# Kernel optimization log

Measured on AMD Instinct MI355X. Metric: run time of the kernel, lower is better.

## Reference

```python
import jax, jax.numpy as jnp
import numpy as np

B, N, D, H, DFF = 4096, 64, 256, 8, 1024
HD = D // H

def _ln(x, g, b):
    m = jnp.mean(x, axis=-1, keepdims=True)
    v = jnp.var(x, axis=-1, keepdims=True)
    return (x - m) / jnp.sqrt(v + 1e-5) * g + b


def setup_inputs() -> dict:
    key = jax.random.key(0)
    ks = jax.random.split(key, 16)
    s = jnp.float32(0.02)
    def rn(k, shape):
        return jax.random.normal(k, shape, dtype=jnp.float32) * s
    d2 = D // 2
    return {
        "x": jax.random.normal(ks[0], (B, N, 1), dtype=jnp.float32),
        "ve_w1": rn(ks[1], (1, d2)), "ve_b1": jnp.zeros((d2,), jnp.float32),
        "ve_w2": rn(ks[2], (d2, D)), "ve_b2": jnp.zeros((D,), jnp.float32),
        "pos_emb": rn(ks[3], (100, D)),
        "attn_in_w": rn(ks[4], (D, 3 * D)), "attn_in_b": jnp.zeros((3 * D,), jnp.float32),
        "attn_out_w": rn(ks[5], (D, D)), "attn_out_b": jnp.zeros((D,), jnp.float32),
        "ffn_w1": rn(ks[6], (D, DFF)), "ffn_b1": jnp.zeros((DFF,), jnp.float32),
        "ffn_w2": rn(ks[7], (DFF, D)), "ffn_b2": jnp.zeros((D,), jnp.float32),
        "ln1_g": jnp.ones((D,), jnp.float32), "ln1_b": jnp.zeros((D,), jnp.float32),
        "ln2_g": jnp.ones((D,), jnp.float32), "ln2_b": jnp.zeros((D,), jnp.float32),
        "rank_emb": rn(ks[8], (100, D)),
        "q_w": rn(ks[9], (D, D)), "q_b": jnp.zeros((D,), jnp.float32),
        "k_w": rn(ks[10], (D, D)), "k_b": jnp.zeros((D,), jnp.float32),
    }


def reference(x, ve_w1, ve_b1, ve_w2, ve_b2, pos_emb, attn_in_w, attn_in_b,
              attn_out_w, attn_out_b, ffn_w1, ffn_b1, ffn_w2, ffn_b2,
              ln1_g, ln1_b, ln2_g, ln2_b, rank_emb, q_w, q_b, k_w, k_b):
    # ---- encode ----
    v = jax.nn.relu(x @ ve_w1 + ve_b1) @ ve_w2 + ve_b2          # [B,N,D]
    h = v + pos_emb[:N][None]                                    # broadcast pos embed
    qkv = h @ attn_in_w + attn_in_b
    q, k, vv = jnp.split(qkv, 3, axis=-1)
    split_heads = lambda t: t.reshape(B, N, H, HD).transpose(0, 2, 1, 3)
    q, k, vv = split_heads(q), split_heads(k), split_heads(vv)
    scores = jnp.einsum('bhqd,bhkd->bhqk', q, k) / jnp.sqrt(jnp.float32(HD))
    attn = jax.nn.softmax(scores, axis=-1)
    ao = jnp.einsum('bhqk,bhkd->bhqd', attn, vv).transpose(0, 2, 1, 3).reshape(B, N, D)
    ao = ao @ attn_out_w + attn_out_b
    h = _ln(h + ao, ln1_g, ln1_b)
    ff = jax.nn.relu(h @ ffn_w1 + ffn_b1) @ ffn_w2 + ffn_b2
    enc = _ln(h + ff, ln2_g, ln2_b)                              # [B,N,D]

    # ---- pointer decode (greedy, coverage mask) ----
    Q = rank_emb[:N] @ q_w + q_b                                 # [N,D] rank queries
    K = enc @ k_w + k_b                                          # [B,N,D]
    base = jnp.einsum('td,bnd->tbn', Q, K)                       # [N,B,N] unmasked logits per rank
    bidx = jnp.arange(B)

    def step(mask, base_t):
        logits_t = jnp.where(mask > 0, base_t, -jnp.inf)         # masked_fill
        chosen = jnp.argmax(logits_t, axis=-1)                   # greedy pick
        mask = mask.at[bidx, chosen].set(0.0)                    # scatter mask update
        return mask, logits_t

    mask0 = jnp.ones((B, N), jnp.float32)
    _, all_logits = jax.lax.scan(step, mask0, base)              # [N,B,N]
    return all_logits.transpose(1, 0, 2)                         # [B,N,N]
```

## Files before the change

kernel.cpp:

```cpp
#include <hip/hip_runtime.h>
#include <math.h>


typedef __attribute__((ext_vector_type(8))) short bf16x8;
typedef __attribute__((ext_vector_type(4))) float f32x4;

#define NEG_FILL (-3.0e38f)

#define U_Q    0
#define U_VE   2048
#define U_QKV  6144
#define U_WO   30720
#define U_F1   38912
#define U_F2   71680
#define U_KW   104448
#define U_TOT  112640

#define SH_H  0
#define SH_A  16384
#define SH_SHORTS 32768
#define FB_FLOATS 4096
#define LDS_BYTES (SH_SHORTS*2 + FB_FLOATS*4)

__device__ __forceinline__ unsigned short f2bf(float f){
  unsigned u = __float_as_uint(f);
  return (unsigned short)((u + 0x7FFFu + ((u>>16)&1u)) >> 16);
}
__device__ __forceinline__ unsigned short f2bt(float f){
  return (unsigned short)(__float_as_uint(f) >> 16);
}
__device__ __forceinline__ float bf2f(unsigned short h){
  return __uint_as_float(((unsigned)h) << 16);
}

#define MFMA(a,b,c) __builtin_amdgcn_mfma_f32_16x16x32_bf16((a),(b),(c),0,0,0)
#define SM_SCALE 0.17677669529663687f
#define PRIO_HI() __builtin_amdgcn_s_setprio(1)
#define PRIO_LO() __builtin_amdgcn_s_setprio(0)

__global__ void __launch_bounds__(256) prep_q(const float* __restrict__ rank_emb,
                                              const float* __restrict__ q_w,
                                              const float* __restrict__ q_b,
                                              short* __restrict__ wsp) {
    int t = blockIdx.x;
    int c = threadIdx.x;
    float acc = q_b[c];
    for (int d = 0; d < 256; d += 4) {
        acc += rank_emb[t*256 + d + 0] * q_w[(d+0)*256 + c]
             + rank_emb[t*256 + d + 1] * q_w[(d+1)*256 + c]
             + rank_emb[t*256 + d + 2] * q_w[(d+2)*256 + c]
             + rank_emb[t*256 + d + 3] * q_w[(d+3)*256 + c];
    }
    int kb = c >> 5, lane = ((c>>3)&3)*16 + (t&15), j = c & 7;
    int u = ((t>>4)*8 + kb)*64 + lane;
    wsp[(U_Q + u)*8 + j] = (short)f2bf(acc);
}

__global__ void __launch_bounds__(256) prep_w(const float* __restrict__ ve_w2,
                                              const float* __restrict__ attn_in_w,
                                              const float* __restrict__ attn_out_w,
                                              const float* __restrict__ ffn_w1,
                                              const float* __restrict__ ffn_w2,
                                              const float* __restrict__ k_w,
                                              short* __restrict__ wsp) {
    int r = blockIdx.x*256 + threadIdx.x;
    const float* w; int N, K, base;
    if (r < 4096)                { w = ve_w2;      N = 256;  K = 128;  base = U_VE;  }
    else if ((r -= 4096)  < 24576) { w = attn_in_w;  N = 768;  K = 256;  base = U_QKV; }
    else if ((r -= 24576) < 8192)  { w = attn_out_w; N = 256;  K = 256;  base = U_WO;  }
    else if ((r -= 8192)  < 32768) { w = ffn_w1;     N = 1024; K = 256;  base = U_F1;  }
    else if ((r -= 32768) < 32768) { w = ffn_w2;     N = 256;  K = 1024; base = U_F2;  }
    else     { r -= 32768;           w = k_w;        N = 256;  K = 256;  base = U_KW;  }
    int KB = K >> 5;
    int lane = r & 63;
    int kb   = (r >> 6) % KB;
    int nt   = r / (64 * KB);
    int n  = nt*16 + (lane & 15);
    int k0 = kb*32 + (lane >> 4)*8;
    bf16x8 hv;
#pragma unroll
    for (int j = 0; j < 8; j++) hv[j] = (short)f2bf(w[(size_t)(k0 + j)*N + n]);
    *(bf16x8*)&wsp[(size_t)(base + r) * 8] = hv;
}

__global__ void __launch_bounds__(512, 4) fused_kernel(
    const float* __restrict__ x,
    const float* __restrict__ ve_w1, const float* __restrict__ ve_b1,
    const float* __restrict__ ve_b2,
    const float* __restrict__ pos_emb,
    const float* __restrict__ attn_in_b,
    const float* __restrict__ attn_out_b,
    const float* __restrict__ ffn_b1, const float* __restrict__ ffn_b2,
    const float* __restrict__ ln1_g, const float* __restrict__ ln1_b,
    const float* __restrict__ ln2_g, const float* __restrict__ ln2_b,
    const float* __restrict__ k_b,
    const short* __restrict__ wsp,
    float* __restrict__ out)
{
    extern __shared__ short sm[];
    float* smf  = (float*)(sm + SH_SHORTS);
    float* SB   = smf;

    const int tid  = threadIdx.x;
    const int b    = blockIdx.x;
    const int w    = tid >> 6;
    const int lane = tid & 63;
    const int quad = lane >> 4;
    const int lcol = lane & 15;

    const bf16x8* wsv = (const bf16x8*)wsp;
    const bf16x8* HFu = (const bf16x8*)&sm[SH_H];
    bf16x8* HFw = (bf16x8*)&sm[SH_H];

#pragma unroll
    for (int i = 0; i < 2; i++) {
        int u = tid + i*512;
        int l3 = u & 63, kb = (u >> 6) & 3, mt = u >> 8;
        int m  = mt*16 + (l3 & 15);
        int k0 = kb*32 + (l3 >> 4)*8;
        float xv = x[b*64 + m];
        bf16x8 hv;
#pragma unroll
        for (int j = 0; j < 8; j++) {
            float f = xv * ve_w1[k0 + j] + ve_b1[k0 + j];
            hv[j] = (short)f2bt(f > 0.f ? f : 0.f);
        }
        *(bf16x8*)&sm[SH_A + u*8] = hv;
    }
    __syncthreads();

    {
        f32x4 acc[2][4];
#pragma unroll
        for (int s = 0; s < 2; s++)
#pragma unroll
            for (int mi = 0; mi < 4; mi++) acc[s][mi] = (f32x4){0.f,0.f,0.f,0.f};
        PRIO_HI();
#pragma unroll
        for (int kb = 0; kb < 4; kb++) {
            bf16x8 bh0 = wsv[U_VE + ((w    )*4+kb)*64 + lane];
            bf16x8 bh1 = wsv[U_VE + ((w + 8)*4+kb)*64 + lane];
#pragma unroll
            for (int mi = 0; mi < 4; mi++) {
                bf16x8 ah = *(const bf16x8*)&sm[SH_A + ((mi*4+kb)*64 + lane)*8];
                acc[0][mi] = MFMA(ah, bh0, acc[0][mi]);
                acc[1][mi] = MFMA(ah, bh1, acc[1][mi]);
            }
        }
        PRIO_LO();
        __syncthreads();
#pragma unroll
        for (int s = 0; s < 2; s++) {
            int n = (w + s*8)*16 + lcol;
#pragma unroll
            for (int mi = 0; mi < 4; mi++)
#pragma unroll
                for (int reg = 0; reg < 4; reg++) {
                    int m = mi*16 + quad*4 + reg;
                    float val = acc[s][mi][reg] + ve_b2[n] + pos_emb[m*256 + n];
                    int kb2 = n >> 5, l2 = ((n>>3)&3)*16 + (m&15), j2 = n & 7;
                    sm[SH_H + ((mi*8 + kb2)*64 + l2)*8 + j2] = (short)f2bt(val);
                }
        }
    }
    __syncthreads();

    f32x4 aoacc[2][4];
#pragma unroll
    for (int s = 0; s < 2; s++)
#pragma unroll
        for (int mi = 0; mi < 4; mi++) aoacc[s][mi] = (f32x4){0.f,0.f,0.f,0.f};

    const int il = w & 3;
    const int eo = il >> 1, ch = il & 1;

    auto qkv_phase = [&](int p) {
        int ntv = 32 + 4*p + il;
        if (w < 4) {
            int ntg = 4*p + il;
            f32x4 acc[4];
#pragma unroll
            for (int mi = 0; mi < 4; mi++) acc[mi] = (f32x4){0.f,0.f,0.f,0.f};
            PRIO_HI();
#pragma unroll
            for (int kb = 0; kb < 8; kb++) {
                bf16x8 bh = wsv[U_QKV + (ntg*8+kb)*64 + lane];
#pragma unroll
                for (int mi = 0; mi < 4; mi++)
                    acc[mi] = MFMA(HFu[(mi*8+kb)*64 + lane], bh, acc[mi]);
            }
            PRIO_LO();
#pragma unroll
            for (int mi = 0; mi < 4; mi++)
#pragma unroll
                for (int reg = 0; reg < 4; reg++) {
                    int m  = mi*16 + quad*4 + reg;
                    int cc = ch*16 + lcol;
                    short hv = (short)f2bt(acc[mi][reg] + attn_in_b[ntg*16 + lcol]);
                    int l2 = ((cc>>3)&3)*16 + (m&15), j2 = cc & 7;
                    sm[SH_A + eo*2048 + (mi*64 + l2)*8 + j2] = hv;
                }
            f32x4 va[2];
            va[0] = (f32x4){0.f,0.f,0.f,0.f}; va[1] = (f32x4){0.f,0.f,0.f,0.f};
            PRIO_HI();
#pragma unroll
            for (int kb = 0; kb < 8; kb++) {
                bf16x8 bh = wsv[U_QKV + (ntv*8+kb)*64 + lane];
                va[0] = MFMA(HFu[(0*8+kb)*64 + lane], bh, va[0]);
                va[1] = MFMA(HFu[(1*8+kb)*64 + lane], bh, va[1]);
            }
            PRIO_LO();
#pragma unroll
            for (int mi = 0; mi < 2; mi++)
#pragma unroll
                for (int reg = 0; reg < 4; reg++) {
                    int m  = mi*16 + quad*4 + reg;
                    int cc = ch*16 + lcol;
                    short hv = (short)f2bt(va[mi][reg] + attn_in_b[ntv*16 + lcol]);
                    int kb2 = m >> 5;
                    int l2 = ((m>>3)&3)*16 + lcol, j2 = m & 7;
                    sm[SH_A + 8192 + eo*2048 + ((ch*2 + kb2)*64 + l2)*8 + j2] = hv;
                }
        } else {
            int ntg = 16 + 4*p + il;
            f32x4 acc[4];
#pragma unroll
            for (int mi = 0; mi < 4; mi++) acc[mi] = (f32x4){0.f,0.f,0.f,0.f};
            PRIO_HI();
#pragma unroll
            for (int kb = 0; kb < 8; kb++) {
                bf16x8 bh = wsv[U_QKV + (ntg*8+kb)*64 + lane];
#pragma unroll
                for (int mi = 0; mi < 4; mi++)
                    acc[mi] = MFMA(HFu[(mi*8+kb)*64 + lane], bh, acc[mi]);
            }
            PRIO_LO();
#pragma unroll
            for (int mi = 0; mi < 4; mi++)
#pragma unroll
                for (int reg = 0; reg < 4; reg++) {
                    int m  = mi*16 + quad*4 + reg;
                    int cc = ch*16 + lcol;
                    short hv = (short)f2bt(acc[mi][reg] + attn_in_b[ntg*16 + lcol]);
                    int l2 = ((cc>>3)&3)*16 + (m&15), j2 = cc & 7;
                    sm[SH_A + 4096 + eo*2048 + ((m>>4)*64 + l2)*8 + j2] = hv;
                }
            f32x4 va[2];
            va[0] = (f32x4){0.f,0.f,0.f,0.f}; va[1] = (f32x4){0.f,0.f,0.f,0.f};
            PRIO_HI();
#pragma unroll
            for (int kb = 0; kb < 8; kb++) {
                bf16x8 bh = wsv[U_QKV + (ntv*8+kb)*64 + lane];
                va[0] = MFMA(HFu[(2*8+kb)*64 + lane], bh, va[0]);
                va[1] = MFMA(HFu[(3*8+kb)*64 + lane], bh, va[1]);
            }
            PRIO_LO();
#pragma unroll
            for (int mi2 = 0; mi2 < 2; mi2++)
#pragma unroll
                for (int reg = 0; reg < 4; reg++) {
                    int m  = (mi2+2)*16 + quad*4 + reg;
                    int cc = ch*16 + lcol;
                    short hv = (short)f2bt(va[mi2][reg] + attn_in_b[ntv*16 + lcol]);
                    int kb2 = m >> 5;
                    int l2 = ((m>>3)&3)*16 + lcol, j2 = m & 7;
                    sm[SH_A + 8192 + eo*2048 + ((ch*2 + kb2)*64 + l2)*8 + j2] = hv;
                }
        }
    };

    auto scores_sm2 = [&]() {
        int e = w >> 2, mi = w & 3;
        bf16x8 ah = *(const bf16x8*)&sm[SH_A + e*2048 + (mi*64 + lane)*8];
        f32x4 sa[4];
        PRIO_HI();
#pragma unroll
        for (int ni = 0; ni < 4; ni++) {
            bf16x8 bh = *(const bf16x8*)&sm[SH_A + 4096 + e*2048 + (ni*64 + lane)*8];
            f32x4 z = (f32x4){0.f,0.f,0.f,0.f};
            sa[ni] = MFMA(ah, bh, z);
        }
        PRIO_LO();
#pragma unroll
        for (int reg = 0; reg < 4; reg++) {
            float v0 = sa[0][reg]*SM_SCALE, v1 = sa[1][reg]*SM_SCALE;
            float v2 = sa[2][reg]*SM_SCALE, v3 = sa[3][reg]*SM_SCALE;
            float mx = fmaxf(fmaxf(v0,v1), fmaxf(v2,v3));
#pragma unroll
            for (int off = 8; off >= 1; off >>= 1) mx = fmaxf(mx, __shfl_xor(mx, off, 64));
            v0 = __expf(v0-mx); v1 = __expf(v1-mx); v2 = __expf(v2-mx); v3 = __expf(v3-mx);
            float s = v0+v1+v2+v3;
#pragma unroll
            for (int off = 8; off >= 1; off >>= 1) s += __shfl_xor(s, off, 64);
            float inv = 1.0f / s;
            float pr[4] = {v0*inv, v1*inv, v2*inv, v3*inv};
            int mr = quad*4 + reg;
#pragma unroll
            for (int ni = 0; ni < 4; ni++) {
                int u  = mi*2 + (ni>>1);
                int l2 = ((ni*2 + (lcol>>3))&3)*16 + mr;
                sm[SH_SHORTS + e*4096 + u*512 + l2*8 + (lcol&7)] = (short)f2bt(pr[ni]);
            }
        }
    };

    auto pv_phase = [&](int e) {
        int mi = w & 3, ni = w >> 2;
        f32x4 pv = (f32x4){0.f,0.f,0.f,0.f};
        PRIO_HI();
#pragma unroll
        for (int kb = 0; kb < 2; kb++) {
            bf16x8 ah = *(const bf16x8*)&sm[SH_SHORTS + e*4096 + ((mi*2+kb)*64 + lane)*8];
            bf16x8 bh = *(const bf16x8*)&sm[SH_A + 8192 + e*2048 + ((ni*2+kb)*64 + lane)*8];
            pv = MFMA(ah, bh, pv);
        }
        PRIO_LO();
#pragma unroll
        for (int reg = 0; reg < 4; reg++) {
            int m = mi*16 + quad*4 + reg;
            int c = ni*16 + lcol;
            int l2 = ((c>>3)&3)*16 + (m&15), j2 = c & 7;
            sm[SH_A + 12288 + e*2048 + (mi*64 + l2)*8 + j2] = (short)f2bt(pv[reg]);
        }
    };

    auto wo_phase = [&](int hh, int e) {
        bf16x8 bh0 = wsv[U_WO + ((w    )*8 + hh)*64 + lane];
        bf16x8 bh1 = wsv[U_WO + ((w + 8)*8 + hh)*64 + lane];
        PRIO_HI();
#pragma unroll
        for (int mi = 0; mi < 4; mi++) {
            bf16x8 ah = *(const bf16x8*)&sm[SH_A + 12288 + e*2048 + (mi*64 + lane)*8];
            aoacc[0][mi] = MFMA(ah, bh0, aoacc[0][mi]);
            aoacc[1][mi] = MFMA(ah, bh1, aoacc[1][mi]);
        }
        PRIO_LO();
    };

    qkv_phase(0);
    __syncthreads();
    for (int p = 0; p < 4; p++) {
        scores_sm2();
        __syncthreads();
        pv_phase(0);  pv_phase(1);
        __syncthreads();
        wo_phase(2*p, 0);  wo_phase(2*p+1, 1);
        if (p < 3) qkv_phase(p+1);
        __syncthreads();
    }

#pragma unroll
    for (int s = 0; s < 2; s++) {
        int n = (w + s*8)*16 + lcol;
#pragma unroll
        for (int mi = 0; mi < 4; mi++)
#pragma unroll
            for (int reg = 0; reg < 4; reg++) {
                int m  = mi*16 + quad*4 + reg;
                int kb2 = n >> 5, l2 = ((n>>3)&3)*16 + (m&15), j2 = n & 7;
                int uu = ((mi*8 + kb2)*64 + l2)*8 + j2;
                float val = bf2f((unsigned short)sm[SH_H + uu]) + aoacc[s][mi][reg] + attn_out_b[n];
                sm[SH_H + uu] = (short)f2bt(val);
            }
    }
    __syncthreads();

    auto layernormFO = [&](const float* __restrict__ g, const float* __restrict__ bt) {
        int m = tid >> 3, kb = tid & 7;
        int ub = ((m>>4)*8 + kb)*64 + (m&15);
        bf16x8 h0 = HFu[ub +  0];
        bf16x8 h1 = HFu[ub + 16];
        bf16x8 h2 = HFu[ub + 32];
        bf16x8 h3 = HFu[ub + 48];
        float v[32];
#pragma unroll
        for (int j = 0; j < 8; j++) {
            v[j]    = bf2f((unsigned short)h0[j]);
            v[8+j]  = bf2f((unsigned short)h1[j]);
            v[16+j] = bf2f((unsigned short)h2[j]);
            v[24+j] = bf2f((unsigned short)h3[j]);
        }
        float sum = 0.f;
#pragma unroll
        for (int i = 0; i < 32; i++) sum += v[i];
#pragma unroll
        for (int off = 4; off >= 1; off >>= 1) sum += __shfl_xor(sum, off, 64);
        float mean = sum * (1.0f/256.0f);
        float s2 = 0.f;
#pragma unroll
        for (int i = 0; i < 32; i++) { float d = v[i] - mean; s2 += d*d; }
#pragma unroll
        for (int off = 4; off >= 1; off >>= 1) s2 += __shfl_xor(s2, off, 64);
        float r = 1.0f / sqrtf(s2 * (1.0f/256.0f) + 1e-5f);
#pragma unroll
        for (int q = 0; q < 4; q++) {
            bf16x8 oh;
#pragma unroll
            for (int j = 0; j < 8; j++) {
                int k = kb*32 + q*8 + j;
                oh[j] = (short)f2bt((v[q*8+j] - mean) * r * g[k] + bt[k]);
            }
            HFw[ub + q*16] = oh;
        }
        __syncthreads();
    };
    layernormFO(ln1_g, ln1_b);

    f32x4 f2acc[2][4];
#pragma unroll
    for (int s = 0; s < 2; s++)
#pragma unroll
        for (int mi = 0; mi < 4; mi++) f2acc[s][mi] = (f32x4){0.f,0.f,0.f,0.f};

    for (int c = 0; c < 4; c++) {
        f32x4 a1[4];
#pragma unroll
        for (int mi = 0; mi < 4; mi++) a1[mi] = (f32x4){0.f,0.f,0.f,0.f};
        PRIO_HI();
#pragma unroll
        for (int kb = 0; kb < 8; kb++) {
            bf16x8 bh = wsv[U_F1 + ((c*16 + w)*8 + kb)*64 + lane];
#pragma unroll
            for (int mi = 0; mi < 4; mi++) {
                bf16x8 ah = HFu[(mi*8+kb)*64 + lane];
                a1[mi] = MFMA(ah, bh, a1[mi]);
            }
        }
        PRIO_LO();
        __syncthreads();
#pragma unroll
        for (int mi = 0; mi < 4; mi++)
#pragma unroll
            for (int reg = 0; reg < 4; reg++) {
                int m = mi*16 + quad*4 + reg;
                int n = (c*16 + w)*16 + lcol;
                float val = a1[mi][reg] + ffn_b1[n];
                val = val > 0.f ? val : 0.f;
                int kk = w*16 + lcol;
                int kb2 = kk >> 5, l2 = ((kk>>3)&3)*16 + (m&15), j2 = kk & 7;
                sm[SH_A + ((mi*8 + kb2)*64 + l2)*8 + j2] = (short)f2bt(val);
            }
#pragma unroll
        for (int mi = 0; mi < 4; mi++) a1[mi] = (f32x4){0.f,0.f,0.f,0.f};
        PRIO_HI();
#pragma unroll
        for (int kb = 0; kb < 8; kb++) {
            bf16x8 bh = wsv[U_F1 + ((c*16 + w + 8)*8 + kb)*64 + lane];
#pragma unroll
            for (int mi = 0; mi < 4; mi++) {
                bf16x8 ah = HFu[(mi*8+kb)*64 + lane];
                a1[mi] = MFMA(ah, bh, a1[mi]);
            }
        }
        PRIO_LO();
#pragma unroll
        for (int mi = 0; mi < 4; mi++)
#pragma unroll
            for (int reg = 0; reg < 4; reg++) {
                int m = mi*16 + quad*4 + reg;
                int n = (c*16 + w + 8)*16 + lcol;
                float val = a1[mi][reg] + ffn_b1[n];
                val = val > 0.f ? val : 0.f;
                int kk = (w + 8)*16 + lcol;
                int kb2 = kk >> 5, l2 = ((kk>>3)&3)*16 + (m&15), j2 = kk & 7;
                sm[SH_A + ((mi*8 + kb2)*64 + l2)*8 + j2] = (short)f2bt(val);
            }
        __syncthreads();
        PRIO_HI();
#pragma unroll 2
        for (int kbl = 0; kbl < 8; kbl++) {
            bf16x8 bh0 = wsv[U_F2 + ((w    )*32 + c*8 + kbl)*64 + lane];
            bf16x8 bh1 = wsv[U_F2 + ((w + 8)*32 + c*8 + kbl)*64 + lane];
#pragma unroll
            for (int mi = 0; mi < 4; mi++) {
                bf16x8 ah = *(const bf16x8*)&sm[SH_A + ((mi*8+kbl)*64 + lane)*8];
                f2acc[0][mi] = MFMA(ah, bh0, f2acc[0][mi]);
                f2acc[1][mi] = MFMA(ah, bh1, f2acc[1][mi]);
            }
        }
        PRIO_LO();
    }
    __syncthreads();
#pragma unroll
    for (int s = 0; s < 2; s++) {
        int n = (w + s*8)*16 + lcol;
#pragma unroll
        for (int mi = 0; mi < 4; mi++)
#pragma unroll
            for (int reg = 0; reg < 4; reg++) {
                int m  = mi*16 + quad*4 + reg;
                int kb2 = n >> 5, l2 = ((n>>3)&3)*16 + (m&15), j2 = n & 7;
                int uu = ((mi*8 + kb2)*64 + l2)*8 + j2;
                float val = bf2f((unsigned short)sm[SH_H + uu]) + f2acc[s][mi][reg] + ffn_b2[n];
                sm[SH_H + uu] = (short)f2bt(val);
            }
    }
    __syncthreads();
    layernormFO(ln2_g, ln2_b);

    {
        f32x4 kacc[2][4];
#pragma unroll
        for (int s = 0; s < 2; s++)
#pragma unroll
            for (int mi = 0; mi < 4; mi++) kacc[s][mi] = (f32x4){0.f,0.f,0.f,0.f};
        PRIO_HI();
#pragma unroll
        for (int kb = 0; kb < 8; kb++) {
            bf16x8 bh0 = wsv[U_KW + ((w    )*8+kb)*64 + lane];
            bf16x8 bh1 = wsv[U_KW + ((w + 8)*8+kb)*64 + lane];
#pragma unroll
            for (int mi = 0; mi < 4; mi++) {
                bf16x8 ah = HFu[(mi*8+kb)*64 + lane];
                kacc[0][mi] = MFMA(ah, bh0, kacc[0][mi]);
                kacc[1][mi] = MFMA(ah, bh1, kacc[1][mi]);
            }
        }
        PRIO_LO();
        __syncthreads();
#pragma unroll
        for (int s = 0; s < 2; s++) {
            int n = (w + s*8)*16 + lcol;
#pragma unroll
            for (int mi = 0; mi < 4; mi++)
#pragma unroll
                for (int reg = 0; reg < 4; reg++) {
                    int m = mi*16 + quad*4 + reg;
                    int nt2 = m >> 4, kb2 = n >> 5;
                    int l2 = ((n>>3)&3)*16 + (m&15), j2 = n & 7;
                    sm[SH_H + ((nt2*8 + kb2)*64 + l2)*8 + j2] =
                        (short)f2bt(kacc[s][mi][reg] + k_b[n]);
                }
        }
    }
    __syncthreads();

#pragma unroll
    for (int it = 0; it < 2; it++) {
        int t = w*2 + it;
        int mi = t >> 2, nt = t & 3;
        f32x4 sacc = (f32x4){0.f,0.f,0.f,0.f};
        PRIO_HI();
#pragma unroll
        for (int kb = 0; kb < 8; kb++) {
            bf16x8 bh = HFu[(nt*8+kb)*64 + lane];
            bf16x8 ah = wsv[U_Q + (mi*8+kb)*64 + lane];
            sacc = MFMA(ah, bh, sacc);
        }
        PRIO_LO();
#pragma unroll
        for (int reg = 0; reg < 4; reg++) {
            int tt = mi*16 + quad*4 + reg;
            int n = nt*16 + lcol;
            SB[tt*64 + (n ^ ((tt&7)<<2))] = sacc[reg];
        }
    }
    __syncthreads();

    if (tid < 64) {
        int ln = tid;
        bool alive = true;
        float* outb = out + (size_t)b * (64*64);
        for (int t = 0; t < 64; t++) {
            float v  = SB[t*64 + (ln ^ ((t&7)<<2))];
            float lv = alive ? v : NEG_FILL;
            outb[t*64 + ln] = lv;
            float bv = lv;
#pragma unroll
            for (int off = 32; off >= 1; off >>= 1)
                bv = fmaxf(bv, __shfl_xor(bv, off, 64));
            unsigned long long mk = __ballot(lv == bv);
            int bi = __ffsll(mk) - 1;
            if (bi == ln) alive = false;
        }
    }
}

extern "C" void kernel_launch(void* const* d_in, const int* in_sizes, int n_in,
                              void* d_out, int out_size, void* d_ws, size_t ws_size,
                              hipStream_t stream) {
    (void)in_sizes; (void)n_in; (void)out_size; (void)ws_size;
    const float* x          = (const float*)d_in[0];
    const float* ve_w1      = (const float*)d_in[1];
    const float* ve_b1      = (const float*)d_in[2];
    const float* ve_w2      = (const float*)d_in[3];
    const float* ve_b2      = (const float*)d_in[4];
    const float* pos_emb    = (const float*)d_in[5];
    const float* attn_in_w  = (const float*)d_in[6];
    const float* attn_in_b  = (const float*)d_in[7];
    const float* attn_out_w = (const float*)d_in[8];
    const float* attn_out_b = (const float*)d_in[9];
    const float* ffn_w1     = (const float*)d_in[10];
    const float* ffn_b1     = (const float*)d_in[11];
    const float* ffn_w2     = (const float*)d_in[12];
    const float* ffn_b2     = (const float*)d_in[13];
    const float* ln1_g      = (const float*)d_in[14];
    const float* ln1_b      = (const float*)d_in[15];
    const float* ln2_g      = (const float*)d_in[16];
    const float* ln2_b      = (const float*)d_in[17];
    const float* rank_emb   = (const float*)d_in[18];
    const float* q_w        = (const float*)d_in[19];
    const float* q_b        = (const float*)d_in[20];
    const float* k_w        = (const float*)d_in[21];
    const float* k_b        = (const float*)d_in[22];
    float* outp = (float*)d_out;
    short* wsp  = (short*)d_ws;

    (void)hipFuncSetAttribute((const void*)fused_kernel,
                              hipFuncAttributeMaxDynamicSharedMemorySize,
                              (int)LDS_BYTES);

    hipLaunchKernelGGL(prep_q, dim3(64), dim3(256), 0, stream, rank_emb, q_w, q_b, wsp);
    hipLaunchKernelGGL(prep_w, dim3(432), dim3(256), 0, stream,
                       ve_w2, attn_in_w, attn_out_w, ffn_w1, ffn_w2, k_w, wsp);
    hipLaunchKernelGGL(fused_kernel, dim3(4096), dim3(512), LDS_BYTES, stream,
                       x, ve_w1, ve_b1, ve_b2, pos_emb,
                       attn_in_b, attn_out_b,
                       ffn_b1, ffn_b2,
                       ln1_g, ln1_b, ln2_g, ln2_b,
                       k_b, (const short*)wsp, outp);
}
```

Measured before the change: 857.8 us.

## Split QKV phase into QK and V parts and software-pipeline attention loop

Splits the QKV projection lambda into separate Q/K and V parts and reorders the per-head-pair loop. The Wo projection of the previous pair and the V projection now run in the scores stage, and the next Q/K projection runs alongside PV. This removes one __syncthreads per iteration (three barriers down to two) and balances work between barriers. It relies on LDS buffer lifetimes lining up so that V and Q/K writes do not overwrite data still being read.

```diff
diff --git a/kernel.cpp b/kernel.cpp
--- a/kernel.cpp
+++ b/kernel.cpp
@@ -173,9 +173,11 @@
 
     const int il = w & 3;
     const int eo = il >> 1, ch = il & 1;
-
-    auto qkv_phase = [&](int p) {
-        int ntv = 32 + 4*p + il;
+    const int mib = (w >> 2) << 1;
+
+    auto qkv_qk = [&](int p) {
+        int cc = ch*16 + lcol;
+        int l2c = ((cc>>3)&3)*16, j2c = cc & 7;
         if (w < 4) {
             int ntg = 4*p + il;
             f32x4 acc[4];
@@ -195,31 +197,8 @@
 #pragma unroll
                 for (int reg = 0; reg < 4; reg++) {
                     int m  = mi*16 + quad*4 + reg;
-                    int cc = ch*16 + lcol;
                     short hv = (short)f2bt(acc[mi][reg] + attn_in_b[ntg*16 + lcol]);
-                    int l2 = ((cc>>3)&3)*16 + (m&15), j2 = cc & 7;
-                    sm[SH_A + eo*2048 + (mi*64 + l2)*8 + j2] = hv;
-                }
-            f32x4 va[2];
-            va[0] = (f32x4){0.f,0.f,0.f,0.f}; va[1] = (f32x4){0.f,0.f,0.f,0.f};
-            PRIO_HI();
-#pragma unroll
-            for (int kb = 0; kb < 8; kb++) {
-                bf16x8 bh = wsv[U_QKV + (ntv*8+kb)*64 + lane];
-                va[0] = MFMA(HFu[(0*8+kb)*64 + lane], bh, va[0]);
-                va[1] = MFMA(HFu[(1*8+kb)*64 + lane], bh, va[1]);
-            }
-            PRIO_LO();
-#pragma unroll
-            for (int mi = 0; mi < 2; mi++)
-#pragma unroll
-                for (int reg = 0; reg < 4; reg++) {
-                    int m  = mi*16 + quad*4 + reg;
-                    int cc = ch*16 + lcol;
-                    short hv = (short)f2bt(va[mi][reg] + attn_in_b[ntv*16 + lcol]);
-                    int kb2 = m >> 5;
-                    int l2 = ((m>>3)&3)*16 + lcol, j2 = m & 7;
-                    sm[SH_A + 8192 + eo*2048 + ((ch*2 + kb2)*64 + l2)*8 + j2] = hv;
+                    sm[SH_A + eo*2048 + (mi*64 + l2c + (m&15))*8 + j2c] = hv;
                 }
         } else {
             int ntg = 16 + 4*p + il;
@@ -240,33 +219,34 @@
 #pragma unroll
                 for (int reg = 0; reg < 4; reg++) {
                     int m  = mi*16 + quad*4 + reg;
-                    int cc = ch*16 + lcol;
                     short hv = (short)f2bt(acc[mi][reg] + attn_in_b[ntg*16 + lcol]);
-                    int l2 = ((cc>>3)&3)*16 + (m&15), j2 = cc & 7;
-                    sm[SH_A + 4096 + eo*2048 + ((m>>4)*64 + l2)*8 + j2] = hv;
+                    sm[SH_A + 4096 + eo*2048 + ((m>>4)*64 + l2c + (m&15))*8 + j2c] = hv;
                 }
-            f32x4 va[2];
-            va[0] = (f32x4){0.f,0.f,0.f,0.f}; va[1] = (f32x4){0.f,0.f,0.f,0.f};
-            PRIO_HI();
-#pragma unroll
-            for (int kb = 0; kb < 8; kb++) {
-                bf16x8 bh = wsv[U_QKV + (ntv*8+kb)*64 + lane];
-                va[0] = MFMA(HFu[(2*8+kb)*64 + lane], bh, va[0]);
-                va[1] = MFMA(HFu[(3*8+kb)*64 + lane], bh, va[1]);
-            }
-            PRIO_LO();
-#pragma unroll
-            for (int mi2 = 0; mi2 < 2; mi2++)
-#pragma unroll
-                for (int reg = 0; reg < 4; reg++) {
-                    int m  = (mi2+2)*16 + quad*4 + reg;
-                    int cc = ch*16 + lcol;
-                    short hv = (short)f2bt(va[mi2][reg] + attn_in_b[ntv*16 + lcol]);
-                    int kb2 = m >> 5;
-                    int l2 = ((m>>3)&3)*16 + lcol, j2 = m & 7;
-                    sm[SH_A + 8192 + eo*2048 + ((ch*2 + kb2)*64 + l2)*8 + j2] = hv;
-                }
-        }
+        }
+    };
+
+    auto qkv_v = [&](int p) {
+        int ntv = 32 + 4*p + il;
+        f32x4 va[2];
+        va[0] = (f32x4){0.f,0.f,0.f,0.f}; va[1] = (f32x4){0.f,0.f,0.f,0.f};
+        PRIO_HI();
+#pragma unroll
+        for (int kb = 0; kb < 8; kb++) {
+            bf16x8 bh = wsv[U_QKV + (ntv*8+kb)*64 + lane];
+            va[0] = MFMA(HFu[((mib+0)*8+kb)*64 + lane], bh, va[0]);
+            va[1] = MFMA(HFu[((mib+1)*8+kb)*64 + lane], bh, va[1]);
+        }
+        PRIO_LO();
+#pragma unroll
+        for (int mi2 = 0; mi2 < 2; mi2++)
+#pragma unroll
+            for (int reg = 0; reg < 4; reg++) {
+                int m  = (mib+mi2)*16 + quad*4 + reg;
+                short hv = (short)f2bt(va[mi2][reg] + attn_in_b[ntv*16 + lcol]);
+                int kb2 = m >> 5;
+                int l2 = ((m>>3)&3)*16 + lcol, j2 = m & 7;
+                sm[SH_A + 8192 + eo*2048 + ((ch*2 + kb2)*64 + l2)*8 + j2] = hv;
+            }
     };
 
     auto scores_sm2 = [&]() {
@@ -337,17 +317,21 @@
         PRIO_LO();
     };
 
-    qkv_phase(0);
+    qkv_qk(0); qkv_v(0);
     __syncthreads();
     for (int p = 0; p < 4; p++) {
         scores_sm2();
+        if (p > 0) {
+            wo_phase(2*(p-1), 0);
+            wo_phase(2*(p-1)+1, 1);
+            qkv_v(p);
+        }
         __syncthreads();
-        pv_phase(0);  pv_phase(1);
+        pv_phase(0); pv_phase(1);
+        if (p < 3) qkv_qk(p+1);
         __syncthreads();
-        wo_phase(2*p, 0);  wo_phase(2*p+1, 1);
-        if (p < 3) qkv_phase(p+1);
-        __syncthreads();
-    }
+    }
+    wo_phase(6, 0); wo_phase(7, 1);
 
 #pragma unroll
     for (int s = 0; s < 2; s++) {
```

Measured after the change: 1.030 ms. 20.0% more time.
